# Kernel optimization log

Hardware: AMD Instinct MI355X
Metric: run time of the kernel (lower is better)

The kernel has to match this reference:

```python
import jax, jax.numpy as jnp
import numpy as np

TEMP = 0.5  # matches temperature init kwarg
EPS = 1e-12  # F.normalize eps


def _l2norm(x):
    # F.normalize(x, dim=1): x / max(||x||, eps)
    n = jnp.linalg.norm(x, axis=1, keepdims=True)
    return x / jnp.maximum(n, EPS)


def setup_inputs() -> dict:
    key = jax.random.key(0)
    k1, k2 = jax.random.split(key)
    B, D = 4096, 256
    return {
        "x_i": jax.random.normal(k1, (B, D), dtype=jnp.float32),
        "x_j": jax.random.normal(k2, (B, D), dtype=jnp.float32),
    }


def reference(x_i, x_j):
    B = x_i.shape[0]
    z = jnp.concatenate([_l2norm(x_i), _l2norm(x_j)], axis=0)  # [2B, D]
    # cosine similarity of normalized rows == matmul (avoids NxNxD broadcast)
    sim = (z @ z.T) / TEMP  # [2B, 2B]
    idx = jnp.arange(B)
    # diagonals at offsets +B and -B = positive pairs
    pos = jnp.concatenate([sim[idx, idx + B], sim[idx + B, idx]])  # [2B]
    exp_sim = jnp.exp(sim)
    # neg = all off-diagonal entries per row (neg_mask = ~eye(2B))
    exp_neg = exp_sim.sum(axis=1) - jnp.exp(jnp.diagonal(sim))  # [2B]
    exp_pos = jnp.exp(pos)
    loss = -jnp.log(exp_pos / (exp_pos + exp_neg))
    return loss.mean()
```

## Files before the change

### kernel.cpp

```cpp
#include <hip/hip_runtime.h>
#include <hip/hip_bf16.h>

typedef __attribute__((ext_vector_type(8))) int   i32x8;
typedef __attribute__((ext_vector_type(4))) int   i32x4;
typedef __attribute__((ext_vector_type(4))) float f32x4;

constexpr int BB = 4096;
constexpr int D  = 256;
constexpr int R2 = 8192;
constexpr int NSPLIT = 32;
constexpr int CPB = R2 / NSPLIT;
constexpr int NG  = CPB / 16;
constexpr int NTRI = NSPLIT * (NSPLIT + 1) / 2;
constexpr int GRID = 512;
constexpr float SCALE = 1.6986436005760381f;
constexpr float E2 = 7.38905609893065f;

__device__ __forceinline__ void async16(const unsigned char* g, unsigned char* l) {
    __builtin_amdgcn_global_load_lds(
        (const __attribute__((address_space(1))) void*)g,
        (__attribute__((address_space(3))) void*)l,
        16, 0, 0);
}

#define MFMA8(A, B, C) \
    __builtin_amdgcn_mfma_scale_f32_16x16x128_f8f6f4((A), (B), (C), 0, 0, 0, 127, 0, 127)

__global__ __launch_bounds__(256) void norm_kernel(const float* __restrict__ xi,
                                                   const float* __restrict__ xj,
                                                   int* __restrict__ z8,
                                                   float* __restrict__ pos,
                                                   float* __restrict__ out) {
    const int wid = threadIdx.x >> 6, lane = threadIdx.x & 63;
    const int k = blockIdx.x * 4 + wid;
    if (blockIdx.x == 0 && threadIdx.x == 0) out[0] = 0.f;
    const float4* a4 = reinterpret_cast<const float4*>(xi + (size_t)k * D);
    const float4* b4 = reinterpret_cast<const float4*>(xj + (size_t)k * D);
    float4 a = a4[lane], b = b4[lane];
    float ssi = a.x*a.x + a.y*a.y + a.z*a.z + a.w*a.w;
    float ssj = b.x*b.x + b.y*b.y + b.z*b.z + b.w*b.w;
    float dot = a.x*b.x + a.y*b.y + a.z*b.z + a.w*b.w;
#pragma unroll
    for (int off = 32; off; off >>= 1) {
        ssi += __shfl_xor(ssi, off);
        ssj += __shfl_xor(ssj, off);
        dot += __shfl_xor(dot, off);
    }
    const float inv_i = 1.0f / fmaxf(sqrtf(ssi), 1e-12f);
    const float inv_j = 1.0f / fmaxf(sqrtf(ssj), 1e-12f);
    const float si = inv_i * SCALE, sj = inv_j * SCALE;
    int pi = __builtin_amdgcn_cvt_pk_fp8_f32(a.x*si, a.y*si, 0, false);
    pi     = __builtin_amdgcn_cvt_pk_fp8_f32(a.z*si, a.w*si, pi, true);
    int pj = __builtin_amdgcn_cvt_pk_fp8_f32(b.x*sj, b.y*sj, 0, false);
    pj     = __builtin_amdgcn_cvt_pk_fp8_f32(b.z*sj, b.w*sj, pj, true);
    z8[(size_t)k * 64 + lane]        = pi;
    z8[(size_t)(k + BB) * 64 + lane] = pj;
    if (lane == 0) pos[k] = dot * inv_i * inv_j * 2.0f;
}

__global__ __launch_bounds__(512, 4) void sim_kernel(const unsigned char* __restrict__ z8,
                                                     float* __restrict__ partial) {
    __shared__ unsigned char tb[CPB * D];
    __shared__ float colws[8][CPB];
    const int tid = threadIdx.x;
    const int wid = tid >> 6, lane = tid & 63;
    const int lrow = lane & 15, quad = lane >> 4;

    for (int task = blockIdx.x; task < NTRI; task += GRID) {
        int t = task, bx = 0;
        while (t >= (NSPLIT - bx)) { t -= (NSPLIT - bx); ++bx; }
        const int by = bx + t;

        const int r0 = bx * 256 + wid * 32;
        const int cbase = by * CPB;

        {
            const int srcg = (tid & 15) ^ ((tid >> 4) & 15);
            const unsigned char* gs = z8 + (size_t)(cbase + (tid >> 4)) * D + srcg * 16;
            unsigned char* ds = tb + tid * 16;
#pragma unroll
            for (int i = 0; i < 8; ++i)
                async16(gs + (size_t)i * 32 * D, ds + i * 8192);
        }

        const unsigned char* abase = z8 + (size_t)(r0 + lrow) * D + quad * 32;
        i32x8 a0k0 = *reinterpret_cast<const i32x8*>(abase             );
        i32x8 a0k1 = *reinterpret_cast<const i32x8*>(abase        + 128);
        i32x8 a1k0 = *reinterpret_cast<const i32x8*>(abase + 16*D      );
        i32x8 a1k1 = *reinterpret_cast<const i32x8*>(abase + 16*D + 128);
        asm volatile("" : "+v"(a0k0), "+v"(a0k1), "+v"(a1k0), "+v"(a1k1));

        f32x4 racc0 = {0.f,0.f,0.f,0.f}, racc1 = {0.f,0.f,0.f,0.f};

        __syncthreads();

        const int pe0 = (quad * 2) ^ lrow;
        const int pe1 = (8 + quad * 2) ^ lrow;
        const unsigned char* rbp = tb + lrow * D;
#pragma unroll 4
        for (int n = 0; n < NG; ++n) {
            const i32x4 lo0 = *reinterpret_cast<const i32x4*>(rbp + pe0*16);
            const i32x4 hi0 = *reinterpret_cast<const i32x4*>(rbp + (pe0^1)*16);
            const i32x4 lo1 = *reinterpret_cast<const i32x4*>(rbp + pe1*16);
            const i32x4 hi1 = *reinterpret_cast<const i32x4*>(rbp + (pe1^1)*16);
            rbp += 16 * D;
            const i32x8 b0 = __builtin_shufflevector(lo0, hi0, 0,1,2,3,4,5,6,7);
            const i32x8 b1 = __builtin_shufflevector(lo1, hi1, 0,1,2,3,4,5,6,7);

            f32x4 c0 = {0.f,0.f,0.f,0.f}, c1 = {0.f,0.f,0.f,0.f};
            c0 = MFMA8(a0k0, b0, c0);  c0 = MFMA8(a0k1, b1, c0);
            c1 = MFMA8(a1k0, b0, c1);  c1 = MFMA8(a1k1, b1, c1);

            const float e0 = __builtin_amdgcn_exp2f(c0[0]);
            const float e1 = __builtin_amdgcn_exp2f(c0[1]);
            const float e2 = __builtin_amdgcn_exp2f(c0[2]);
            const float e3 = __builtin_amdgcn_exp2f(c0[3]);
            const float e4 = __builtin_amdgcn_exp2f(c1[0]);
            const float e5 = __builtin_amdgcn_exp2f(c1[1]);
            const float e6 = __builtin_amdgcn_exp2f(c1[2]);
            const float e7 = __builtin_amdgcn_exp2f(c1[3]);
            racc0[0] += e0;  racc0[1] += e1;  racc0[2] += e2;  racc0[3] += e3;
            racc1[0] += e4;  racc1[1] += e5;  racc1[2] += e6;  racc1[3] += e7;

            float cs = ((e0 + e1) + (e2 + e3)) + ((e4 + e5) + (e6 + e7));
            cs += __shfl_xor(cs, 16);
            cs += __shfl_xor(cs, 32);
            if (quad == 0) colws[wid][n * 16 + lrow] = cs;
        }

#define REDUCE_STORE(RV, M)                                                     \
        {                                                                       \
            _Pragma("unroll")                                                   \
            for (int j = 0; j < 4; ++j) {                                       \
                float v = (RV)[j];                                              \
                v += __shfl_xor(v, 1);                                          \
                v += __shfl_xor(v, 2);                                          \
                v += __shfl_xor(v, 4);                                          \
                v += __shfl_xor(v, 8);                                          \
                if (lrow == 0)                                                  \
                    partial[(size_t)by * R2 + r0 + (M)*16 + quad*4 + j] = v;    \
            }                                                                   \
        }
        REDUCE_STORE(racc0, 0)
        REDUCE_STORE(racc1, 1)
#undef REDUCE_STORE

        __syncthreads();
        if (bx != by && tid < CPB) {
            float s = 0.f;
#pragma unroll
            for (int w = 0; w < 8; ++w) s += colws[w][tid];
            partial[(size_t)bx * R2 + cbase + tid] = s;
        }
    }
}

__global__ __launch_bounds__(256) void reduce_kernel(const float* __restrict__ partial,
                                                     const float* __restrict__ pos,
                                                     float* __restrict__ out) {
    __shared__ float wsum[4];
    const int tid = threadIdx.x;
    const int r = blockIdx.x * 256 + tid;
    float S = 0.f;
#pragma unroll
    for (int s = 0; s < NSPLIT; ++s) S += partial[(size_t)s * R2 + r];
    const float p = pos[r & (BB - 1)];
    float lsum = __logf(__expf(p) + S - E2) - p;
#pragma unroll
    for (int off = 32; off; off >>= 1) lsum += __shfl_xor(lsum, off);
    if ((tid & 63) == 0) wsum[tid >> 6] = lsum;
    __syncthreads();
    if (tid == 0) {
        float t = wsum[0] + wsum[1] + wsum[2] + wsum[3];
        atomicAdd(out, t * (1.0f / (float)R2));
    }
}

extern "C" void kernel_launch(void* const* d_in, const int* in_sizes, int n_in,
                              void* d_out, int out_size, void* d_ws, size_t ws_size,
                              hipStream_t stream) {
    (void)in_sizes; (void)n_in; (void)out_size; (void)ws_size;
    const float* xi = (const float*)d_in[0];
    const float* xj = (const float*)d_in[1];
    float* out = (float*)d_out;

    unsigned char* z8 = (unsigned char*)d_ws;
    float* partial = (float*)((char*)d_ws + (size_t)R2 * D);
    float* pos     = (float*)((char*)d_ws + (size_t)R2 * D + (size_t)NSPLIT*R2*4);

    norm_kernel<<<BB / 4, 256, 0, stream>>>(xi, xj, (int*)z8, pos, out);
    sim_kernel<<<GRID, 512, 0, stream>>>(z8, partial);
    reduce_kernel<<<R2 / 256, 256, 0, stream>>>(partial, pos, out);
}
```

Baseline: 85.01 us.

## Use 4-wave sim blocks with 64 rows per wave to reuse B tiles

Halves the sim kernel block to 256 threads, with each wave now covering 64 rows (four 16-row MFMA tiles) instead of 32. Every B fragment read from LDS feeds twice as many MFMAs, and the column-sum LDS scratch and its reduction shrink to four waves. The cost is more registers per thread for the A fragments and accumulators, and fewer waves per block to hide the LDS load and the exp latency. Occupancy may change as a result.

```diff
diff --git a/kernel.cpp b/kernel.cpp
--- a/kernel.cpp
+++ b/kernel.cpp
@@ -58,10 +58,10 @@
     if (lane == 0) pos[k] = dot * inv_i * inv_j * 2.0f;
 }
 
-__global__ __launch_bounds__(512, 4) void sim_kernel(const unsigned char* __restrict__ z8,
+__global__ __launch_bounds__(256, 2) void sim_kernel(const unsigned char* __restrict__ z8,
                                                      float* __restrict__ partial) {
     __shared__ unsigned char tb[CPB * D];
-    __shared__ float colws[8][CPB];
+    __shared__ float colws[4][CPB];
     const int tid = threadIdx.x;
     const int wid = tid >> 6, lane = tid & 63;
     const int lrow = lane & 15, quad = lane >> 4;
@@ -71,7 +71,7 @@
         while (t >= (NSPLIT - bx)) { t -= (NSPLIT - bx); ++bx; }
         const int by = bx + t;
 
-        const int r0 = bx * 256 + wid * 32;
+        const int r0 = bx * 256 + wid * 64;
         const int cbase = by * CPB;
 
         {
@@ -79,8 +79,8 @@
             const unsigned char* gs = z8 + (size_t)(cbase + (tid >> 4)) * D + srcg * 16;
             unsigned char* ds = tb + tid * 16;
 #pragma unroll
-            for (int i = 0; i < 8; ++i)
-                async16(gs + (size_t)i * 32 * D, ds + i * 8192);
+            for (int i = 0; i < 16; ++i)
+                async16(gs + (size_t)i * 16 * D, ds + i * 4096);
         }
 
         const unsigned char* abase = z8 + (size_t)(r0 + lrow) * D + quad * 32;
@@ -88,9 +88,15 @@
         i32x8 a0k1 = *reinterpret_cast<const i32x8*>(abase        + 128);
         i32x8 a1k0 = *reinterpret_cast<const i32x8*>(abase + 16*D      );
         i32x8 a1k1 = *reinterpret_cast<const i32x8*>(abase + 16*D + 128);
-        asm volatile("" : "+v"(a0k0), "+v"(a0k1), "+v"(a1k0), "+v"(a1k1));
+        i32x8 a2k0 = *reinterpret_cast<const i32x8*>(abase + 32*D      );
+        i32x8 a2k1 = *reinterpret_cast<const i32x8*>(abase + 32*D + 128);
+        i32x8 a3k0 = *reinterpret_cast<const i32x8*>(abase + 48*D      );
+        i32x8 a3k1 = *reinterpret_cast<const i32x8*>(abase + 48*D + 128);
+        asm volatile("" : "+v"(a0k0), "+v"(a0k1), "+v"(a1k0), "+v"(a1k1),
+                          "+v"(a2k0), "+v"(a2k1), "+v"(a3k0), "+v"(a3k1));
 
         f32x4 racc0 = {0.f,0.f,0.f,0.f}, racc1 = {0.f,0.f,0.f,0.f};
+        f32x4 racc2 = {0.f,0.f,0.f,0.f}, racc3 = {0.f,0.f,0.f,0.f};
 
         __syncthreads();
 
@@ -108,21 +114,35 @@
             const i32x8 b1 = __builtin_shufflevector(lo1, hi1, 0,1,2,3,4,5,6,7);
 
             f32x4 c0 = {0.f,0.f,0.f,0.f}, c1 = {0.f,0.f,0.f,0.f};
+            f32x4 c2 = {0.f,0.f,0.f,0.f}, c3 = {0.f,0.f,0.f,0.f};
             c0 = MFMA8(a0k0, b0, c0);  c0 = MFMA8(a0k1, b1, c0);
             c1 = MFMA8(a1k0, b0, c1);  c1 = MFMA8(a1k1, b1, c1);
-
-            const float e0 = __builtin_amdgcn_exp2f(c0[0]);
-            const float e1 = __builtin_amdgcn_exp2f(c0[1]);
-            const float e2 = __builtin_amdgcn_exp2f(c0[2]);
-            const float e3 = __builtin_amdgcn_exp2f(c0[3]);
-            const float e4 = __builtin_amdgcn_exp2f(c1[0]);
-            const float e5 = __builtin_amdgcn_exp2f(c1[1]);
-            const float e6 = __builtin_amdgcn_exp2f(c1[2]);
-            const float e7 = __builtin_amdgcn_exp2f(c1[3]);
-            racc0[0] += e0;  racc0[1] += e1;  racc0[2] += e2;  racc0[3] += e3;
-            racc1[0] += e4;  racc1[1] += e5;  racc1[2] += e6;  racc1[3] += e7;
-
-            float cs = ((e0 + e1) + (e2 + e3)) + ((e4 + e5) + (e6 + e7));
+            c2 = MFMA8(a2k0, b0, c2);  c2 = MFMA8(a2k1, b1, c2);
+            c3 = MFMA8(a3k0, b0, c3);  c3 = MFMA8(a3k1, b1, c3);
+
+            const float e0  = __builtin_amdgcn_exp2f(c0[0]);
+            const float e1  = __builtin_amdgcn_exp2f(c0[1]);
+            const float e2  = __builtin_amdgcn_exp2f(c0[2]);
+            const float e3  = __builtin_amdgcn_exp2f(c0[3]);
+            const float e4  = __builtin_amdgcn_exp2f(c1[0]);
+            const float e5  = __builtin_amdgcn_exp2f(c1[1]);
+            const float e6  = __builtin_amdgcn_exp2f(c1[2]);
+            const float e7  = __builtin_amdgcn_exp2f(c1[3]);
+            const float e8  = __builtin_amdgcn_exp2f(c2[0]);
+            const float e9  = __builtin_amdgcn_exp2f(c2[1]);
+            const float e10 = __builtin_amdgcn_exp2f(c2[2]);
+            const float e11 = __builtin_amdgcn_exp2f(c2[3]);
+            const float e12 = __builtin_amdgcn_exp2f(c3[0]);
+            const float e13 = __builtin_amdgcn_exp2f(c3[1]);
+            const float e14 = __builtin_amdgcn_exp2f(c3[2]);
+            const float e15 = __builtin_amdgcn_exp2f(c3[3]);
+            racc0[0] += e0;   racc0[1] += e1;   racc0[2] += e2;   racc0[3] += e3;
+            racc1[0] += e4;   racc1[1] += e5;   racc1[2] += e6;   racc1[3] += e7;
+            racc2[0] += e8;   racc2[1] += e9;   racc2[2] += e10;  racc2[3] += e11;
+            racc3[0] += e12;  racc3[1] += e13;  racc3[2] += e14;  racc3[3] += e15;
+
+            float cs = (((e0 + e1) + (e2 + e3)) + ((e4 + e5) + (e6 + e7)))
+                     + (((e8 + e9) + (e10 + e11)) + ((e12 + e13) + (e14 + e15)));
             cs += __shfl_xor(cs, 16);
             cs += __shfl_xor(cs, 32);
             if (quad == 0) colws[wid][n * 16 + lrow] = cs;
@@ -143,13 +163,13 @@
         }
         REDUCE_STORE(racc0, 0)
         REDUCE_STORE(racc1, 1)
+        REDUCE_STORE(racc2, 2)
+        REDUCE_STORE(racc3, 3)
 #undef REDUCE_STORE
 
         __syncthreads();
-        if (bx != by && tid < CPB) {
-            float s = 0.f;
-#pragma unroll
-            for (int w = 0; w < 8; ++w) s += colws[w][tid];
+        if (bx != by) {
+            float s = colws[0][tid] + colws[1][tid] + colws[2][tid] + colws[3][tid];
             partial[(size_t)bx * R2 + cbase + tid] = s;
         }
     }
@@ -189,6 +209,6 @@
     float* pos     = (float*)((char*)d_ws + (size_t)R2 * D + (size_t)NSPLIT*R2*4);
 
     norm_kernel<<<BB / 4, 256, 0, stream>>>(xi, xj, (int*)z8, pos, out);
-    sim_kernel<<<GRID, 512, 0, stream>>>(z8, partial);
+    sim_kernel<<<GRID, 256, 0, stream>>>(z8, partial);
     reduce_kernel<<<R2 / 256, 256, 0, stream>>>(partial, pos, out);
 }
```

Result: slower. 88.43 us (+4.0%).
